# Optimization experiments

Measured on AMD Instinct MI355X. Metric: run time of the kernel, lower is better.

Reference implementation:

```python
import jax, jax.numpy as jnp
import numpy as np

# Deformable-DETR style 4-level pyramid (H, W) per level; num_keys = 13294
SPATIAL_SHAPES = np.array([[100, 100], [50, 50], [25, 25], [13, 13]], dtype=np.int32)


def setup_inputs() -> dict:
    key = jax.random.key(0)
    k1, k2, k3 = jax.random.split(key, 3)
    bs, nh, D = 2, 8, 32          # batch, heads, per-head embed dim
    L, P = 4, 4                   # levels, points
    K = int((SPATIAL_SHAPES[:, 0] * SPATIAL_SHAPES[:, 1]).sum())  # 13294 keys
    Q = K                         # encoder self-attention: queries == keys
    value = jax.random.normal(k1, (bs, K, nh, D), jnp.float32)
    sampling_locations = jax.random.uniform(k2, (bs, Q, nh, L, P, 2), jnp.float32)
    aw = jax.random.uniform(k3, (bs, Q, nh, L, P), jnp.float32)
    attention_weights = aw / aw.sum(axis=(3, 4), keepdims=True)
    return {
        "value": value,
        "value_spatial_shapes": jnp.asarray(SPATIAL_SHAPES),
        "sampling_locations": sampling_locations,
        "attention_weights": attention_weights,
    }


def _bilinear_sample(v, grid, H, W):
    """grid_sample(mode='bilinear', padding_mode='zeros', align_corners=False).
    v:    (bs, nh, H*W, D)
    grid: (bs, nh, Q, P, 2) with coords in [-1, 1], last dim = (x, y)
    returns (bs, nh, Q, P, D)
    """
    # unnormalize (align_corners=False): ((g+1)*size - 1) / 2
    x = (grid[..., 0] + 1.0) * (W * 0.5) - 0.5
    y = (grid[..., 1] + 1.0) * (H * 0.5) - 0.5
    x0 = jnp.floor(x)
    y0 = jnp.floor(y)
    dx = x - x0
    dy = y - y0
    x0i = x0.astype(jnp.int32)
    y0i = y0.astype(jnp.int32)

    def gather(xi, yi):
        valid = (xi >= 0) & (xi < W) & (yi >= 0) & (yi < H)
        idx = jnp.clip(yi, 0, H - 1) * W + jnp.clip(xi, 0, W - 1)
        b, h, q, p = idx.shape
        g = jnp.take_along_axis(v, idx.reshape(b, h, q * p, 1), axis=2)
        g = g.reshape(b, h, q, p, v.shape[-1])
        return g * valid[..., None].astype(v.dtype)

    v00 = gather(x0i, y0i)
    v01 = gather(x0i + 1, y0i)
    v10 = gather(x0i, y0i + 1)
    v11 = gather(x0i + 1, y0i + 1)
    w00 = ((1.0 - dx) * (1.0 - dy))[..., None]
    w01 = (dx * (1.0 - dy))[..., None]
    w10 = ((1.0 - dx) * dy)[..., None]
    w11 = (dx * dy)[..., None]
    return v00 * w00 + v01 * w01 + v10 * w10 + v11 * w11


def reference(value, value_spatial_shapes, sampling_locations, attention_weights):
    shapes = np.asarray(value_spatial_shapes)  # static level shapes
    bs, K, nh, D = value.shape
    _, Q, _, L, P, _ = sampling_locations.shape
    grids = 2.0 * sampling_locations - 1.0                 # (bs,Q,nh,L,P,2)
    grids = jnp.transpose(grids, (0, 2, 1, 3, 4, 5))       # (bs,nh,Q,L,P,2)
    aw = jnp.transpose(attention_weights, (0, 2, 1, 3, 4)) # (bs,nh,Q,L,P)
    out = jnp.zeros((bs, nh, Q, D), value.dtype)
    start = 0
    for lvl in range(shapes.shape[0]):
        H, W = int(shapes[lvl, 0]), int(shapes[lvl, 1])
        v_l = jnp.transpose(value[:, start:start + H * W], (0, 2, 1, 3))  # (bs,nh,HW,D)
        s = _bilinear_sample(v_l, grids[:, :, :, lvl], H, W)              # (bs,nh,Q,P,D)
        out = out + jnp.einsum('bhqpd,bhqp->bhqd', s, aw[:, :, :, lvl])
        start += H * W
    # (bs,nh,Q,D) -> (bs,Q,nh*D): head-major channel order, matching torch view
    return jnp.transpose(out, (0, 2, 1, 3)).reshape(bs, Q, nh * D)
```

## Files before the change

### kernel.cpp

```cpp
#include <hip/hip_runtime.h>


#define BS 2
#define NH 8
#define DD 32
#define LL 4
#define PP 4
#define QQ 13294
#define KK 13294
#define LPG 8
#define GPB 32

typedef float f32x2 __attribute__((ext_vector_type(2)));
typedef float f32x4 __attribute__((ext_vector_type(4)));

__global__ __launch_bounds__(256) void msda_fwd_kernel(
    const f32x4* __restrict__ value4,
    const f32x2* __restrict__ loc2,
    const float* __restrict__ aw,
    f32x4*       __restrict__ out4)
{
    constexpr int Hs[4]     = {100, 50, 25, 13};
    constexpr int Ws[4]     = {100, 50, 25, 13};
    constexpr int starts[4] = {0, 10000, 12500, 13125};

    const int gid  = blockIdx.x * GPB + (threadIdx.x >> 3);
    const int lane = threadIdx.x & (LPG - 1);

    const int q  = gid % QQ;
    const int bh = gid / QQ;
    const int h  = bh % NH;
    const int b  = bh / NH;

    const size_t lp_base = ((size_t)(b * QQ + q) * NH + h) * (LL * PP);
    const f32x2* lp = loc2 + lp_base;
    const float* wp = aw   + lp_base;

    const f32x4* vbase = value4 + ((size_t)b * KK * NH + h) * (DD / 4) + lane;

    f32x4 acc = {0.0f, 0.0f, 0.0f, 0.0f};

    #pragma unroll
    for (int l = 0; l < LL; ++l) {
        const int H = Hs[l], W = Ws[l];
        const float fH = (float)H, fW = (float)W;
        #pragma unroll
        for (int p = 0; p < PP; ++p) {
            const int s = l * PP + p;
            const f32x2 lxy = __builtin_nontemporal_load(&lp[s]);
            const float w   = __builtin_nontemporal_load(&wp[s]);

            const float x = lxy.x * fW - 0.5f;
            const float y = lxy.y * fH - 0.5f;
            const float x0f = floorf(x), y0f = floorf(y);
            const float dx = x - x0f, dy = y - y0f;
            const int x0 = (int)x0f, y0 = (int)y0f;
            const int x1 = x0 + 1,  y1 = y0 + 1;

            const float mx0 = ((unsigned)x0 < (unsigned)W) ? 1.0f : 0.0f;
            const float mx1 = ((unsigned)x1 < (unsigned)W) ? 1.0f : 0.0f;
            const float my0 = ((unsigned)y0 < (unsigned)H) ? 1.0f : 0.0f;
            const float my1 = ((unsigned)y1 < (unsigned)H) ? 1.0f : 0.0f;

            const int cx0 = min(max(x0, 0), W - 1);
            const int cx1 = min(max(x1, 0), W - 1);
            const int cy0 = min(max(y0, 0), H - 1);
            const int cy1 = min(max(y1, 0), H - 1);

            const float w00 = (1.0f - dx) * (1.0f - dy) * w * mx0 * my0;
            const float w01 = dx * (1.0f - dy) * w * mx1 * my0;
            const float w10 = (1.0f - dx) * dy * w * mx0 * my1;
            const float w11 = dx * dy * w * mx1 * my1;

            const int r0 = starts[l] + cy0 * W;
            const int r1 = starts[l] + cy1 * W;
            const f32x4 v00 = vbase[(size_t)(r0 + cx0) * (NH * DD / 4)];
            const f32x4 v01 = vbase[(size_t)(r0 + cx1) * (NH * DD / 4)];
            const f32x4 v10 = vbase[(size_t)(r1 + cx0) * (NH * DD / 4)];
            const f32x4 v11 = vbase[(size_t)(r1 + cx1) * (NH * DD / 4)];

            acc.x = fmaf(w00, v00.x, acc.x);
            acc.y = fmaf(w00, v00.y, acc.y);
            acc.z = fmaf(w00, v00.z, acc.z);
            acc.w = fmaf(w00, v00.w, acc.w);
            acc.x = fmaf(w01, v01.x, acc.x);
            acc.y = fmaf(w01, v01.y, acc.y);
            acc.z = fmaf(w01, v01.z, acc.z);
            acc.w = fmaf(w01, v01.w, acc.w);
            acc.x = fmaf(w10, v10.x, acc.x);
            acc.y = fmaf(w10, v10.y, acc.y);
            acc.z = fmaf(w10, v10.z, acc.z);
            acc.w = fmaf(w10, v10.w, acc.w);
            acc.x = fmaf(w11, v11.x, acc.x);
            acc.y = fmaf(w11, v11.y, acc.y);
            acc.z = fmaf(w11, v11.z, acc.z);
            acc.w = fmaf(w11, v11.w, acc.w);
        }
    }

    __builtin_nontemporal_store(acc, &out4[((size_t)(b * QQ + q) * NH + h) * (DD / 4) + lane]);
}

extern "C" void kernel_launch(void* const* d_in, const int* in_sizes, int n_in,
                              void* d_out, int out_size, void* d_ws, size_t ws_size,
                              hipStream_t stream) {
    const f32x4* value4 = (const f32x4*)d_in[0];
    const f32x2* loc2   = (const f32x2*)d_in[2];
    const float* aw     = (const float*)d_in[3];
    f32x4*       out4   = (f32x4*)d_out;

    const int total_groups = BS * NH * QQ;
    const int blocks = total_groups / GPB;

    msda_fwd_kernel<<<blocks, 256, 0, stream>>>(value4, loc2, aw, out4);
}
```

Baseline: 131.3 us.

## Process two queries per thread group with vectorized location and weight loads

Each 8-lane group now handles two queries (q and q+QQ/2) for the same batch and head, which halves the grid and doubles the independent gather chains per thread. Sampling locations and attention weights are read as 16-byte vectors per level instead of per-point 8-byte and 4-byte loads. A launch-bounds occupancy hint of 4 is also added. The goal is more memory-level parallelism and fewer load instructions, at the cost of higher register pressure and fewer waves in flight.

```diff
diff --git a/kernel.cpp b/kernel.cpp
--- a/kernel.cpp
+++ b/kernel.cpp
@@ -4,113 +4,135 @@
 #define BS 2
 #define NH 8
 #define DD 32
-#define LL 4
-#define PP 4
 #define QQ 13294
 #define KK 13294
+#define QH 6647
 #define LPG 8
 #define GPB 32
+#define NPAIR (BS * NH * QH)
+#define NWG ((NPAIR + GPB - 1) / GPB)
+#define KSTR (NH * DD / 4)
 
-typedef float f32x2 __attribute__((ext_vector_type(2)));
 typedef float f32x4 __attribute__((ext_vector_type(4)));
 
-__global__ __launch_bounds__(256) void msda_fwd_kernel(
+__device__ __forceinline__ void level_chain(const f32x4* __restrict__ vbase,
+                                            const f32x4 lv0, const f32x4 lv1,
+                                            const f32x4 wv,
+                                            const int H, const int W, const int start,
+                                            f32x4& acc)
+{
+    const float fH = (float)H, fW = (float)W;
+    #pragma unroll
+    for (int p = 0; p < 4; ++p) {
+        const f32x4 lvp = (p < 2) ? lv0 : lv1;
+        const float lx = lvp[(p & 1) * 2 + 0];
+        const float ly = lvp[(p & 1) * 2 + 1];
+        const float w  = wv[p];
+
+        const float x = lx * fW - 0.5f;
+        const float y = ly * fH - 0.5f;
+        const float x0f = floorf(x), y0f = floorf(y);
+        const float dx = x - x0f, dy = y - y0f;
+        const int x0 = (int)x0f, y0 = (int)y0f;
+        const int x1 = x0 + 1,  y1 = y0 + 1;
+
+        const float mx0 = ((unsigned)x0 < (unsigned)W) ? 1.0f : 0.0f;
+        const float mx1 = ((unsigned)x1 < (unsigned)W) ? 1.0f : 0.0f;
+        const float my0 = ((unsigned)y0 < (unsigned)H) ? 1.0f : 0.0f;
+        const float my1 = ((unsigned)y1 < (unsigned)H) ? 1.0f : 0.0f;
+
+        const int cx0 = min(max(x0, 0), W - 1);
+        const int cx1 = min(max(x1, 0), W - 1);
+        const int cy0 = min(max(y0, 0), H - 1);
+        const int cy1 = min(max(y1, 0), H - 1);
+
+        const float w00 = (1.0f - dx) * (1.0f - dy) * w * mx0 * my0;
+        const float w01 = dx * (1.0f - dy) * w * mx1 * my0;
+        const float w10 = (1.0f - dx) * dy * w * mx0 * my1;
+        const float w11 = dx * dy * w * mx1 * my1;
+
+        const int r0 = start + cy0 * W;
+        const int r1 = start + cy1 * W;
+        const f32x4 v00 = vbase[(size_t)(r0 + cx0) * KSTR];
+        const f32x4 v01 = vbase[(size_t)(r0 + cx1) * KSTR];
+        const f32x4 v10 = vbase[(size_t)(r1 + cx0) * KSTR];
+        const f32x4 v11 = vbase[(size_t)(r1 + cx1) * KSTR];
+
+        acc.x = fmaf(w00, v00.x, acc.x);
+        acc.y = fmaf(w00, v00.y, acc.y);
+        acc.z = fmaf(w00, v00.z, acc.z);
+        acc.w = fmaf(w00, v00.w, acc.w);
+        acc.x = fmaf(w01, v01.x, acc.x);
+        acc.y = fmaf(w01, v01.y, acc.y);
+        acc.z = fmaf(w01, v01.z, acc.z);
+        acc.w = fmaf(w01, v01.w, acc.w);
+        acc.x = fmaf(w10, v10.x, acc.x);
+        acc.y = fmaf(w10, v10.y, acc.y);
+        acc.z = fmaf(w10, v10.z, acc.z);
+        acc.w = fmaf(w10, v10.w, acc.w);
+        acc.x = fmaf(w11, v11.x, acc.x);
+        acc.y = fmaf(w11, v11.y, acc.y);
+        acc.z = fmaf(w11, v11.z, acc.z);
+        acc.w = fmaf(w11, v11.w, acc.w);
+    }
+}
+
+__global__ __launch_bounds__(256, 4) void msda_fwd_kernel(
     const f32x4* __restrict__ value4,
-    const f32x2* __restrict__ loc2,
-    const float* __restrict__ aw,
+    const f32x4* __restrict__ locv,
+    const f32x4* __restrict__ awv,
     f32x4*       __restrict__ out4)
 {
     constexpr int Hs[4]     = {100, 50, 25, 13};
     constexpr int Ws[4]     = {100, 50, 25, 13};
     constexpr int starts[4] = {0, 10000, 12500, 13125};
 
-    const int gid  = blockIdx.x * GPB + (threadIdx.x >> 3);
+    const int pair = blockIdx.x * GPB + (threadIdx.x >> 3);
     const int lane = threadIdx.x & (LPG - 1);
+    if (pair >= NPAIR) return;
 
-    const int q  = gid % QQ;
-    const int bh = gid / QQ;
+    const int qh = pair % QH;
+    const int bh = pair / QH;
     const int h  = bh % NH;
     const int b  = bh / NH;
 
-    const size_t lp_base = ((size_t)(b * QQ + q) * NH + h) * (LL * PP);
-    const f32x2* lp = loc2 + lp_base;
-    const float* wp = aw   + lp_base;
+    const size_t giA = ((size_t)(b * QQ + qh) * NH + h);
+    const size_t giB = ((size_t)(b * QQ + qh + QH) * NH + h);
+
+    const f32x4* lpA = locv + giA * 8;
+    const f32x4* wpA = awv  + giA * 4;
+    const f32x4* lpB = locv + giB * 8;
+    const f32x4* wpB = awv  + giB * 4;
 
     const f32x4* vbase = value4 + ((size_t)b * KK * NH + h) * (DD / 4) + lane;
 
-    f32x4 acc = {0.0f, 0.0f, 0.0f, 0.0f};
+    f32x4 accA = {0.f, 0.f, 0.f, 0.f};
+    f32x4 accB = {0.f, 0.f, 0.f, 0.f};
 
     #pragma unroll
-    for (int l = 0; l < LL; ++l) {
-        const int H = Hs[l], W = Ws[l];
-        const float fH = (float)H, fW = (float)W;
-        #pragma unroll
-        for (int p = 0; p < PP; ++p) {
-            const int s = l * PP + p;
-            const f32x2 lxy = __builtin_nontemporal_load(&lp[s]);
-            const float w   = __builtin_nontemporal_load(&wp[s]);
+    for (int l = 0; l < 4; ++l) {
+        const f32x4 lvA0 = __builtin_nontemporal_load(&lpA[2 * l + 0]);
+        const f32x4 lvA1 = __builtin_nontemporal_load(&lpA[2 * l + 1]);
+        const f32x4 wvA  = __builtin_nontemporal_load(&wpA[l]);
+        const f32x4 lvB0 = __builtin_nontemporal_load(&lpB[2 * l + 0]);
+        const f32x4 lvB1 = __builtin_nontemporal_load(&lpB[2 * l + 1]);
+        const f32x4 wvB  = __builtin_nontemporal_load(&wpB[l]);
 
-            const float x = lxy.x * fW - 0.5f;
-            const float y = lxy.y * fH - 0.5f;
-            const float x0f = floorf(x), y0f = floorf(y);
-            const float dx = x - x0f, dy = y - y0f;
-            const int x0 = (int)x0f, y0 = (int)y0f;
-            const int x1 = x0 + 1,  y1 = y0 + 1;
-
-            const float mx0 = ((unsigned)x0 < (unsigned)W) ? 1.0f : 0.0f;
-            const float mx1 = ((unsigned)x1 < (unsigned)W) ? 1.0f : 0.0f;
-            const float my0 = ((unsigned)y0 < (unsigned)H) ? 1.0f : 0.0f;
-            const float my1 = ((unsigned)y1 < (unsigned)H) ? 1.0f : 0.0f;
-
-            const int cx0 = min(max(x0, 0), W - 1);
-            const int cx1 = min(max(x1, 0), W - 1);
-            const int cy0 = min(max(y0, 0), H - 1);
-            const int cy1 = min(max(y1, 0), H - 1);
-
-            const float w00 = (1.0f - dx) * (1.0f - dy) * w * mx0 * my0;
-            const float w01 = dx * (1.0f - dy) * w * mx1 * my0;
-            const float w10 = (1.0f - dx) * dy * w * mx0 * my1;
-            const float w11 = dx * dy * w * mx1 * my1;
-
-            const int r0 = starts[l] + cy0 * W;
-            const int r1 = starts[l] + cy1 * W;
-            const f32x4 v00 = vbase[(size_t)(r0 + cx0) * (NH * DD / 4)];
-            const f32x4 v01 = vbase[(size_t)(r0 + cx1) * (NH * DD / 4)];
-            const f32x4 v10 = vbase[(size_t)(r1 + cx0) * (NH * DD / 4)];
-            const f32x4 v11 = vbase[(size_t)(r1 + cx1) * (NH * DD / 4)];
-
-            acc.x = fmaf(w00, v00.x, acc.x);
-            acc.y = fmaf(w00, v00.y, acc.y);
-            acc.z = fmaf(w00, v00.z, acc.z);
-            acc.w = fmaf(w00, v00.w, acc.w);
-            acc.x = fmaf(w01, v01.x, acc.x);
-            acc.y = fmaf(w01, v01.y, acc.y);
-            acc.z = fmaf(w01, v01.z, acc.z);
-            acc.w = fmaf(w01, v01.w, acc.w);
-            acc.x = fmaf(w10, v10.x, acc.x);
-            acc.y = fmaf(w10, v10.y, acc.y);
-            acc.z = fmaf(w10, v10.z, acc.z);
-            acc.w = fmaf(w10, v10.w, acc.w);
-            acc.x = fmaf(w11, v11.x, acc.x);
-            acc.y = fmaf(w11, v11.y, acc.y);
-            acc.z = fmaf(w11, v11.z, acc.z);
-            acc.w = fmaf(w11, v11.w, acc.w);
-        }
+        level_chain(vbase, lvA0, lvA1, wvA, Hs[l], Ws[l], starts[l], accA);
+        level_chain(vbase, lvB0, lvB1, wvB, Hs[l], Ws[l], starts[l], accB);
     }
 
-    __builtin_nontemporal_store(acc, &out4[((size_t)(b * QQ + q) * NH + h) * (DD / 4) + lane]);
+    __builtin_nontemporal_store(accA, &out4[giA * (DD / 4) + lane]);
+    __builtin_nontemporal_store(accB, &out4[giB * (DD / 4) + lane]);
 }
 
 extern "C" void kernel_launch(void* const* d_in, const int* in_sizes, int n_in,
                               void* d_out, int out_size, void* d_ws, size_t ws_size,
                               hipStream_t stream) {
     const f32x4* value4 = (const f32x4*)d_in[0];
-    const f32x2* loc2   = (const f32x2*)d_in[2];
-    const float* aw     = (const float*)d_in[3];
+    const f32x4* locv   = (const f32x4*)d_in[2];
+    const f32x4* awv    = (const f32x4*)d_in[3];
     f32x4*       out4   = (f32x4*)d_out;
 
-    const int total_groups = BS * NH * QQ;
-    const int blocks = total_groups / GPB;
-
-    msda_fwd_kernel<<<blocks, 256, 0, stream>>>(value4, loc2, aw, out4);
+    msda_fwd_kernel<<<NWG, 256, 0, stream>>>(value4, locv, awv, out4);
 }
```

Result: slower. 141.7 us (+7.9%).

## Repack value to head-major layout in workspace and vectorize location/weight loads

Applied to the files above, without the earlier changes.

Adds a pre-pass kernel that transposes value from (b,k,h,d) to (b,h,k,d) in the workspace, so each head's keys sit contiguously at a 128-byte stride instead of 1 KB. This is meant to give the bilinear gathers better cache-line and TLB locality. The sampling locations and attention weights are now fetched as 16-byte vectors per level rather than scalar or 8-byte loads, and launch bounds now request 4 blocks per SM. The cost is an extra full read and write of value (about 27 MB) on every call plus a second kernel launch; if the workspace is too small it falls back to the original layout.

```diff
diff --git a/kernel.cpp b/kernel.cpp
--- a/kernel.cpp
+++ b/kernel.cpp
@@ -4,20 +4,36 @@
 #define BS 2
 #define NH 8
 #define DD 32
-#define LL 4
-#define PP 4
 #define QQ 13294
 #define KK 13294
 #define LPG 8
 #define GPB 32
+#define NWG 6647
+#define NV4 (BS * KK * NH * (DD / 4))
+#define RWG (NV4 / 256)
 
-typedef float f32x2 __attribute__((ext_vector_type(2)));
 typedef float f32x4 __attribute__((ext_vector_type(4)));
 
-__global__ __launch_bounds__(256) void msda_fwd_kernel(
+__global__ __launch_bounds__(256) void msda_repack_kernel(
     const f32x4* __restrict__ value4,
-    const f32x2* __restrict__ loc2,
-    const float* __restrict__ aw,
+    f32x4*       __restrict__ packed4)
+{
+    const int idx = blockIdx.x * 256 + threadIdx.x;
+    const int d4 = idx & 7;
+    const int t  = idx >> 3;
+    const int h  = t % NH;
+    const int bk = t / NH;
+    const int k  = bk % KK;
+    const int b  = bk / KK;
+    const f32x4 v = __builtin_nontemporal_load(&value4[idx]);
+    packed4[(((size_t)(b * NH + h) * KK) + k) * 8 + d4] = v;
+}
+
+template <int KSTRIDE>
+__global__ __launch_bounds__(256, 4) void msda_fwd_kernel(
+    const f32x4* __restrict__ val4,
+    const f32x4* __restrict__ locv,
+    const f32x4* __restrict__ awv,
     f32x4*       __restrict__ out4)
 {
     constexpr int Hs[4]     = {100, 50, 25, 13};
@@ -32,26 +48,33 @@
     const int h  = bh % NH;
     const int b  = bh / NH;
 
-    const size_t lp_base = ((size_t)(b * QQ + q) * NH + h) * (LL * PP);
-    const f32x2* lp = loc2 + lp_base;
-    const float* wp = aw   + lp_base;
+    const size_t lg = (size_t)(b * QQ + q) * NH + h;
+    const f32x4* lp = locv + lg * 8;
+    const f32x4* wp = awv  + lg * 4;
 
-    const f32x4* vbase = value4 + ((size_t)b * KK * NH + h) * (DD / 4) + lane;
+    const f32x4* vbase = (KSTRIDE == 8)
+        ? val4 + ((size_t)(b * NH + h) * KK) * 8 + lane
+        : val4 + ((size_t)b * KK * NH + h) * (DD / 4) + lane;
 
-    f32x4 acc = {0.0f, 0.0f, 0.0f, 0.0f};
+    f32x4 acc = {0.f, 0.f, 0.f, 0.f};
 
     #pragma unroll
-    for (int l = 0; l < LL; ++l) {
+    for (int l = 0; l < 4; ++l) {
         const int H = Hs[l], W = Ws[l];
         const float fH = (float)H, fW = (float)W;
+        const f32x4 lv0 = __builtin_nontemporal_load(&lp[2 * l + 0]);
+        const f32x4 lv1 = __builtin_nontemporal_load(&lp[2 * l + 1]);
+        const f32x4 wvv = __builtin_nontemporal_load(&wp[l]);
+
         #pragma unroll
-        for (int p = 0; p < PP; ++p) {
-            const int s = l * PP + p;
-            const f32x2 lxy = __builtin_nontemporal_load(&lp[s]);
-            const float w   = __builtin_nontemporal_load(&wp[s]);
+        for (int p = 0; p < 4; ++p) {
+            const f32x4 lvp = (p < 2) ? lv0 : lv1;
+            const float lx = lvp[(p & 1) * 2 + 0];
+            const float ly = lvp[(p & 1) * 2 + 1];
+            const float w  = wvv[p];
 
-            const float x = lxy.x * fW - 0.5f;
-            const float y = lxy.y * fH - 0.5f;
+            const float x = lx * fW - 0.5f;
+            const float y = ly * fH - 0.5f;
             const float x0f = floorf(x), y0f = floorf(y);
             const float dx = x - x0f, dy = y - y0f;
             const int x0 = (int)x0f, y0 = (int)y0f;
@@ -74,10 +97,10 @@
 
             const int r0 = starts[l] + cy0 * W;
             const int r1 = starts[l] + cy1 * W;
-            const f32x4 v00 = vbase[(size_t)(r0 + cx0) * (NH * DD / 4)];
-            const f32x4 v01 = vbase[(size_t)(r0 + cx1) * (NH * DD / 4)];
-            const f32x4 v10 = vbase[(size_t)(r1 + cx0) * (NH * DD / 4)];
-            const f32x4 v11 = vbase[(size_t)(r1 + cx1) * (NH * DD / 4)];
+            const f32x4 v00 = vbase[(size_t)(r0 + cx0) * KSTRIDE];
+            const f32x4 v01 = vbase[(size_t)(r0 + cx1) * KSTRIDE];
+            const f32x4 v10 = vbase[(size_t)(r1 + cx0) * KSTRIDE];
+            const f32x4 v11 = vbase[(size_t)(r1 + cx1) * KSTRIDE];
 
             acc.x = fmaf(w00, v00.x, acc.x);
             acc.y = fmaf(w00, v00.y, acc.y);
@@ -98,19 +121,23 @@
         }
     }
 
-    __builtin_nontemporal_store(acc, &out4[((size_t)(b * QQ + q) * NH + h) * (DD / 4) + lane]);
+    __builtin_nontemporal_store(acc, &out4[lg * (DD / 4) + lane]);
 }
 
 extern "C" void kernel_launch(void* const* d_in, const int* in_sizes, int n_in,
                               void* d_out, int out_size, void* d_ws, size_t ws_size,
                               hipStream_t stream) {
     const f32x4* value4 = (const f32x4*)d_in[0];
-    const f32x2* loc2   = (const f32x2*)d_in[2];
-    const float* aw     = (const float*)d_in[3];
+    const f32x4* locv   = (const f32x4*)d_in[2];
+    const f32x4* awv    = (const f32x4*)d_in[3];
     f32x4*       out4   = (f32x4*)d_out;
 
-    const int total_groups = BS * NH * QQ;
-    const int blocks = total_groups / GPB;
-
-    msda_fwd_kernel<<<blocks, 256, 0, stream>>>(value4, loc2, aw, out4);
+    const size_t need = (size_t)NV4 * sizeof(f32x4);
+    if (ws_size >= need) {
+        f32x4* packed4 = (f32x4*)d_ws;
+        msda_repack_kernel<<<RWG, 256, 0, stream>>>(value4, packed4);
+        msda_fwd_kernel<8><<<NWG, 256, 0, stream>>>(packed4, locv, awv, out4);
+    } else {
+        msda_fwd_kernel<NH * DD / 4><<<NWG, 256, 0, stream>>>(value4, locv, awv, out4);
+    }
 }
```

After: 141.1 us. 1.07x slower.
